# Kernel tuning notes

Hardware: AMD Instinct MI355X
Metric: run time of the kernel (lower is better)

Reference implementation:

```python
import jax, jax.numpy as jnp
import numpy as np

T, N, D, H = 12, 50000, 32, 128  # timesteps, nodes, input_dim, hidden_dim
DEC_STEPS = 7


def setup_inputs() -> dict:
    key = jax.random.key(0)
    ks = jax.random.split(key, 10)
    w = lambda k, shape, s=0.1: jax.random.normal(k, shape, dtype=jnp.float32) * s
    return {
        "x": jax.random.normal(ks[0], (T, N, D), dtype=jnp.float32),
        # input_encoder: Linear(D, H)
        "enc_W": w(ks[1], (H, D)), "enc_b": jnp.zeros((H,), jnp.float32),
        # encoder LSTM (1 layer), PyTorch gate order i,f,g,o
        "Wih_e": w(ks[2], (4 * H, H)), "Whh_e": w(ks[3], (4 * H, H)),
        "bih_e": jnp.zeros((4 * H,), jnp.float32), "bhh_e": jnp.zeros((4 * H,), jnp.float32),
        # decoder LSTM (1 layer)
        "Wih_d": w(ks[4], (4 * H, H)), "Whh_d": w(ks[5], (4 * H, H)),
        "bih_d": jnp.zeros((4 * H,), jnp.float32), "bhh_d": jnp.zeros((4 * H,), jnp.float32),
        # head: fc1(H -> H//2), fc2(H//2 -> 1)
        "fc1_W": w(ks[6], (H // 2, H)), "fc1_b": jnp.zeros((H // 2,), jnp.float32),
        "fc2_W": w(ks[7], (1, H // 2)), "fc2_b": jnp.zeros((1,), jnp.float32),
    }


def _lstm_cell(x, h, c, Wih, Whh, b):
    # PyTorch LSTM gate layout: [i, f, g, o] along the 4H axis.
    z = x @ Wih.T + h @ Whh.T + b
    i, f, g, o = jnp.split(z, 4, axis=-1)
    c = jax.nn.sigmoid(f) * c + jax.nn.sigmoid(i) * jnp.tanh(g)
    h = jax.nn.sigmoid(o) * jnp.tanh(c)
    return h, c


def reference(x, enc_W, enc_b, Wih_e, Whh_e, bih_e, bhh_e,
              Wih_d, Whh_d, bih_d, bhh_d, fc1_W, fc1_b, fc2_W, fc2_b):
    t, n, d = x.shape
    h_dim = enc_W.shape[0]
    # input_encoder applied to all nodes/timesteps at once: [T,N,H]
    enc_seq = jax.nn.relu(jnp.einsum('tnd,hd->tnh', x, enc_W) + enc_b)

    h0 = jnp.zeros((n, h_dim), x.dtype)
    c0 = jnp.zeros((n, h_dim), x.dtype)
    b_e = bih_e + bhh_e

    def enc_step(carry, xt):
        h, c = carry
        h, c = _lstm_cell(xt, h, c, Wih_e, Whh_e, b_e)
        return (h, c), None

    (h, c), _ = jax.lax.scan(enc_step, (h0, c0), enc_seq)

    # decoder input = last encoder output (fixed across all 7 steps, as in source)
    d_in = h
    b_d = bih_d + bhh_d

    def dec_step(carry, _):
        hd, cd = carry
        hd, cd = _lstm_cell(d_in, hd, cd, Wih_d, Whh_d, b_d)
        out = jax.nn.relu(hd @ fc1_W.T + fc1_b)  # dropout is identity at inference
        pred = out @ fc2_W.T + fc2_b             # [N, 1]
        return (hd, cd), pred[:, 0]

    _, preds = jax.lax.scan(dec_step, (h, c), None, length=DEC_STEPS)  # [7, N]
    return preds.T  # [N, 7]
```

## Files before the change

kernel.cpp:

```cpp
#include <hip/hip_runtime.h>

#define TSTEPS 12
#define NNODES 50000
#define DIN 32
#define HDIM 128
#define DECS 7

#define N80 53
#define NB 768
#define RTMAX 5
#define ROWSMAX 80

#define HS 136
#define XS 36
#define ESZ (ROWSMAX * HS)

typedef _Float16 half_t;
typedef _Float16 half8 __attribute__((ext_vector_type(8)));
typedef float float4_ __attribute__((ext_vector_type(4)));

#define WS_FLOAT_OFF 548864

#define SM_BYTES 157440
#define E_OFF 69120
#define H_OFF 112640
#define PRED_OFF 156160
#define ZX_PLANE_H 20480

#if __has_builtin(__builtin_amdgcn_exp2f)
#define EXP2F __builtin_amdgcn_exp2f
#else
#define EXP2F exp2f
#endif
#if __has_builtin(__builtin_amdgcn_rcpf)
#define RCPF __builtin_amdgcn_rcpf
#else
#define RCPF(x) (1.0f / (x))
#endif

__device__ __forceinline__ float lstm_one(float i, float f, float g, float o, float& c) {
    float ai = EXP2F(-1.44269504f * i);
    float af = EXP2F(-1.44269504f * f);
    float ag = EXP2F(-2.88539008f * g);
    float ao = EXP2F(-1.44269504f * o);
    float sf = RCPF(1.0f + af);
    float ig = (1.0f - ag) * RCPF((1.0f + ai) * (1.0f + ag));
    c = fmaf(sf, c, ig);
    float ac = EXP2F(-2.88539008f * c);
    return (1.0f - ac) * RCPF((1.0f + ao) * (1.0f + ac));
}

__global__ void prep_all_k(const float* __restrict__ Wih_e, const float* __restrict__ Whh_e,
                           const float* __restrict__ Wih_d, const float* __restrict__ Whh_d,
                           const float* __restrict__ enc_W, const float* __restrict__ fc1_W,
                           const float* __restrict__ bih_e, const float* __restrict__ bhh_e,
                           const float* __restrict__ bih_d, const float* __restrict__ bhh_d,
                           half_t* __restrict__ wsh, float* __restrict__ be, float* __restrict__ bd) {
    int tid = blockIdx.x * blockDim.x + threadIdx.x;
    if (tid < 262144) {
        int r = tid >> 16;
        int t = tid & 65535;
        const float* src = (r == 0) ? Wih_e : (r == 1) ? Whh_e : (r == 2) ? Wih_d : Whh_d;
        int j    = t & 7;
        int lane = (t >> 3) & 63;
        int rest = t >> 9;
        int kb   = rest & 3;
        int ct   = rest >> 2;
        int row  = ct * 16 + (lane & 15);
        int col  = kb * 32 + ((lane >> 4) << 3) + j;
        wsh[tid] = (half_t)src[row * 128 + col];
    } else if (tid < 266240) {
        int t    = tid - 262144;
        int j    = t & 7;
        int lane = (t >> 3) & 63;
        int ct   = t >> 9;
        int row  = ct * 16 + (lane & 15);
        int col  = ((lane >> 4) << 3) + j;
        wsh[tid] = (half_t)enc_W[row * 32 + col];
    } else if (tid < 274432) {
        int t    = tid - 266240;
        int j    = t & 7;
        int lane = (t >> 3) & 63;
        int rest = t >> 9;
        int kb   = rest & 3;
        int ct   = rest >> 2;
        int row  = ct * 16 + (lane & 15);
        int col  = kb * 32 + ((lane >> 4) << 3) + j;
        wsh[tid] = (half_t)fc1_W[row * 128 + col];
    } else if (tid < 274944) {
        int t = tid - 274432;
        be[t] = bih_e[t] + bhh_e[t];
        bd[t] = bih_d[t] + bhh_d[t];
    }
}

__device__ __forceinline__ void lstm_step(
    const half_t* __restrict__ eA, const half_t* __restrict__ hA, half_t* __restrict__ hOut,
    const half8 (&wfi)[4][4], const half8 (&wfh)[4][4],
    const float bR[4], float (&cS)[RTMAX][4],
    int w, int q, int l15, int RT) {
#pragma unroll
    for (int rt = 0; rt < RTMAX; ++rt) {
        if (rt < RT) {
            float4_ acc[4];
#pragma unroll
            for (int g = 0; g < 4; ++g) {
                float b = bR[g];
                acc[g][0] = b; acc[g][1] = b; acc[g][2] = b; acc[g][3] = b;
            }
#pragma unroll
            for (int kb = 0; kb < 4; ++kb) {
                half8 ae = *(const half8*)(eA + (rt * 16 + l15) * HS + kb * 32 + q * 8);
                half8 ah = *(const half8*)(hA + (rt * 16 + l15) * HS + kb * 32 + q * 8);
#pragma unroll
                for (int g = 0; g < 4; ++g) {
                    acc[g] = __builtin_amdgcn_mfma_f32_16x16x32_f16(ae, wfi[g][kb], acc[g], 0, 0, 0);
                    acc[g] = __builtin_amdgcn_mfma_f32_16x16x32_f16(ah, wfh[g][kb], acc[g], 0, 0, 0);
                }
            }
#pragma unroll
            for (int r = 0; r < 4; ++r) {
                float h = lstm_one(acc[0][r], acc[1][r], acc[2][r], acc[3][r], cS[rt][r]);
                hOut[(rt * 16 + q * 4 + r) * HS + w * 16 + l15] = (half_t)h;
            }
        }
    }
}

__device__ __forceinline__ void lstm_step_dec(
    const half_t* __restrict__ zx, const half_t* __restrict__ hA, half_t* __restrict__ hOut,
    const half8 (&wfh)[4][4], float (&cS)[RTMAX][4],
    int w, int q, int l15, int lane, int RT) {
#pragma unroll
    for (int rt = 0; rt < RTMAX; ++rt) {
        if (rt < RT) {
            const half_t* p0 = zx + ((w * RTMAX + rt) * 64 + lane) * 8;
            half8 z0 = *(const half8*)p0;
            half8 z1 = *(const half8*)(p0 + ZX_PLANE_H);
            float4_ acc[4];
#pragma unroll
            for (int r = 0; r < 4; ++r) {
                acc[0][r] = (float)z0[r];
                acc[1][r] = (float)z0[4 + r];
                acc[2][r] = (float)z1[r];
                acc[3][r] = (float)z1[4 + r];
            }
#pragma unroll
            for (int kb = 0; kb < 4; ++kb) {
                half8 ah = *(const half8*)(hA + (rt * 16 + l15) * HS + kb * 32 + q * 8);
#pragma unroll
                for (int g = 0; g < 4; ++g)
                    acc[g] = __builtin_amdgcn_mfma_f32_16x16x32_f16(ah, wfh[g][kb], acc[g], 0, 0, 0);
            }
#pragma unroll
            for (int r = 0; r < 4; ++r) {
                float h = lstm_one(acc[0][r], acc[1][r], acc[2][r], acc[3][r], cS[rt][r]);
                hOut[(rt * 16 + q * 4 + r) * HS + w * 16 + l15] = (half_t)h;
            }
        }
    }
}

__device__ __forceinline__ void enc_proj(
    const half_t* __restrict__ xa, half_t* __restrict__ eOut,
    half8 encWf, float benc, int t, int w, int q, int l15, int RT) {
#pragma unroll
    for (int rt = 0; rt < RTMAX; ++rt) {
        if (rt < RT) {
            half8 af = *(const half8*)(xa + ((t * ROWSMAX) + rt * 16 + l15) * XS + q * 8);
            float4_ a;
            a[0] = benc; a[1] = benc; a[2] = benc; a[3] = benc;
            a = __builtin_amdgcn_mfma_f32_16x16x32_f16(af, encWf, a, 0, 0, 0);
#pragma unroll
            for (int r = 0; r < 4; ++r) {
                float v = a[r];
                v = v > 0.f ? v : 0.f;
                eOut[(rt * 16 + q * 4 + r) * HS + w * 16 + l15] = (half_t)v;
            }
        }
    }
}

__global__ __launch_bounds__(512, 2) void seq2seq_main_k(
    const float* __restrict__ x,
    const float* __restrict__ enc_b,
    const float* __restrict__ fc1_b,
    const float* __restrict__ fc2_W,
    const float* __restrict__ fc2_b,
    const half_t* __restrict__ wsh,
    const float* __restrict__ be,
    const float* __restrict__ bd,
    float* __restrict__ out) {
    __shared__ __align__(16) char smem[SM_BYTES];
    half_t* xa = (half_t*)smem;
    half_t* eB = (half_t*)(smem + E_OFF);
    half_t* hB = (half_t*)(smem + H_OFF);
    float (*pred)[ROWSMAX] = (float(*)[ROWSMAX])(smem + PRED_OFF);
    half_t* zx = (half_t*)smem;

    const int tid  = threadIdx.x;
    const int lane = tid & 63;
    const int w    = tid >> 6;
    const int q    = lane >> 4;
    const int l15  = lane & 15;
    const int bid  = blockIdx.x;
    const int big  = (bid < N80);
    const int RT   = big ? 5 : 4;
    const int rows = RT << 4;
    const int n0   = big ? bid * 80 : (N80 * 80 + (bid - N80) * 64);

    const half_t* WihE  = wsh;
    const half_t* WhhE  = wsh + 65536;
    const half_t* WihD  = wsh + 131072;
    const half_t* WhhD  = wsh + 196608;
    const half_t* encWp = wsh + 262144;
    const half_t* fc1p  = wsh + 266240;

    float beR[4], bdR[4];
#pragma unroll
    for (int g = 0; g < 4; ++g) {
        int col = g * 128 + w * 16 + l15;
        beR[g] = be[col];
        bdR[g] = bd[col];
    }
    float benc = enc_b[w * 16 + l15];

    for (int it = 0; it < 8; ++it) {
        int unit = tid + it * 512;
        if (unit >= TSTEPS * ROWSMAX * 4) break;
        int t    = unit / (ROWSMAX * 4);
        int rest = unit - t * (ROWSMAX * 4);
        int row  = rest >> 2;
        int c0   = (rest & 3) * 8;
        if (row < rows) {
            const float* p = x + ((size_t)t * NNODES + (n0 + row)) * DIN + c0;
            float4_ a0 = *(const float4_*)p;
            float4_ a1 = *(const float4_*)(p + 4);
            half8 hv;
            hv[0] = (half_t)a0[0]; hv[1] = (half_t)a0[1]; hv[2] = (half_t)a0[2]; hv[3] = (half_t)a0[3];
            hv[4] = (half_t)a1[0]; hv[5] = (half_t)a1[1]; hv[6] = (half_t)a1[2]; hv[7] = (half_t)a1[3];
            *(half8*)(xa + (t * ROWSMAX + row) * XS + c0) = hv;
        }
    }

    for (int i = tid; i < rows * HS; i += 512) hB[i] = (half_t)0.0f;

    float c_reg[RTMAX][4];
#pragma unroll
    for (int rt = 0; rt < RTMAX; ++rt)
#pragma unroll
        for (int r = 0; r < 4; ++r) c_reg[rt][r] = 0.0f;

    half8 wfi[4][4], wfh[4][4];
#pragma unroll
    for (int g = 0; g < 4; ++g)
#pragma unroll
        for (int kb = 0; kb < 4; ++kb) {
            int ct = g * 8 + w;
            wfi[g][kb] = *(const half8*)(WihE + ((size_t)(ct * 4 + kb) * 64 + lane) * 8);
            wfh[g][kb] = *(const half8*)(WhhE + ((size_t)(ct * 4 + kb) * 64 + lane) * 8);
        }
    half8 encWf = *(const half8*)(encWp + (size_t)w * 512 + lane * 8);

    __syncthreads();

    enc_proj(xa, eB, encWf, benc, 0, w, q, l15, RT);
    __syncthreads();

    int cur = 0;
    for (int t = 0; t < TSTEPS; ++t) {
        lstm_step(eB + (t & 1) * ESZ, hB + cur * ESZ, hB + (cur ^ 1) * ESZ,
                  wfi, wfh, beR, c_reg, w, q, l15, RT);
        if (t + 1 < TSTEPS)
            enc_proj(xa, eB + ((t & 1) ^ 1) * ESZ, encWf, benc, t + 1, w, q, l15, RT);
        __syncthreads();
        cur ^= 1;
    }

#pragma unroll
    for (int g = 0; g < 4; ++g)
#pragma unroll
        for (int kb = 0; kb < 4; ++kb) {
            int ct = g * 8 + w;
            wfi[g][kb] = *(const half8*)(WihD + ((size_t)(ct * 4 + kb) * 64 + lane) * 8);
            wfh[g][kb] = *(const half8*)(WhhD + ((size_t)(ct * 4 + kb) * 64 + lane) * 8);
        }
    half8 fc1f[4];
#pragma unroll
    for (int kb = 0; kb < 4; ++kb)
        fc1f[kb] = *(const half8*)(fc1p + ((size_t)((w & 3) * 4 + kb) * 64 + lane) * 8);
    float bf1 = fc1_b[(w & 3) * 16 + l15];
    float wf2 = fc2_W[(w & 3) * 16 + l15];
    float bf2 = fc2_b[0];
    const int gg = w >> 2;

    {
        const half_t* hfin = hB + cur * ESZ;
#pragma unroll
        for (int rt = 0; rt < RTMAX; ++rt) {
            if (rt < RT) {
                float4_ acc[4];
#pragma unroll
                for (int g = 0; g < 4; ++g) {
                    float b = bdR[g];
                    acc[g][0] = b; acc[g][1] = b; acc[g][2] = b; acc[g][3] = b;
                }
#pragma unroll
                for (int kb = 0; kb < 4; ++kb) {
                    half8 ah = *(const half8*)(hfin + (rt * 16 + l15) * HS + kb * 32 + q * 8);
#pragma unroll
                    for (int g = 0; g < 4; ++g)
                        acc[g] = __builtin_amdgcn_mfma_f32_16x16x32_f16(ah, wfi[g][kb], acc[g], 0, 0, 0);
                }
                half8 z0, z1;
#pragma unroll
                for (int r = 0; r < 4; ++r) {
                    z0[r]     = (half_t)acc[0][r];
                    z0[4 + r] = (half_t)acc[1][r];
                    z1[r]     = (half_t)acc[2][r];
                    z1[4 + r] = (half_t)acc[3][r];
                }
                half_t* p0 = zx + ((w * RTMAX + rt) * 64 + lane) * 8;
                *(half8*)p0 = z0;
                *(half8*)(p0 + ZX_PLANE_H) = z1;
            }
        }
    }

    for (int s = 0; s < DECS; ++s) {
        lstm_step_dec(zx, hB + cur * ESZ, hB + (cur ^ 1) * ESZ, wfh, c_reg, w, q, l15, lane, RT);
        cur ^= 1;
        __syncthreads();
        const half_t* hc = hB + cur * ESZ;
#pragma unroll
        for (int rp = 0; rp < 3; ++rp) {
            int rt = gg + rp * 2;
            if (rt < RT) {
                float4_ hacc;
                hacc[0] = bf1; hacc[1] = bf1; hacc[2] = bf1; hacc[3] = bf1;
#pragma unroll
                for (int kb = 0; kb < 4; ++kb) {
                    half8 af = *(const half8*)(hc + (rt * 16 + l15) * HS + kb * 32 + q * 8);
                    hacc = __builtin_amdgcn_mfma_f32_16x16x32_f16(af, fc1f[kb], hacc, 0, 0, 0);
                }
#pragma unroll
                for (int r = 0; r < 4; ++r) {
                    float v = hacc[r];
                    v = v > 0.f ? v : 0.f;
                    v *= wf2;
                    v += __shfl_xor(v, 1, 64);
                    v += __shfl_xor(v, 2, 64);
                    v += __shfl_xor(v, 4, 64);
                    v += __shfl_xor(v, 8, 64);
                    if (l15 == 0) pred[w & 3][rt * 16 + q * 4 + r] = v;
                }
            }
        }
        __syncthreads();
        if (tid < rows) {
            float sum = pred[0][tid] + pred[1][tid] + pred[2][tid] + pred[3][tid] + bf2;
            out[(size_t)(n0 + tid) * DECS + s] = sum;
        }
    }
}

extern "C" void kernel_launch(void* const* d_in, const int* in_sizes, int n_in,
                              void* d_out, int out_size, void* d_ws, size_t ws_size,
                              hipStream_t stream) {
    (void)in_sizes; (void)n_in; (void)out_size; (void)ws_size;
    const float* x     = (const float*)d_in[0];
    const float* enc_W = (const float*)d_in[1];
    const float* enc_b = (const float*)d_in[2];
    const float* Wih_e = (const float*)d_in[3];
    const float* Whh_e = (const float*)d_in[4];
    const float* bih_e = (const float*)d_in[5];
    const float* bhh_e = (const float*)d_in[6];
    const float* Wih_d = (const float*)d_in[7];
    const float* Whh_d = (const float*)d_in[8];
    const float* bih_d = (const float*)d_in[9];
    const float* bhh_d = (const float*)d_in[10];
    const float* fc1_W = (const float*)d_in[11];
    const float* fc1_b = (const float*)d_in[12];
    const float* fc2_W = (const float*)d_in[13];
    const float* fc2_b = (const float*)d_in[14];

    half_t* wsh = (half_t*)d_ws;
    float*  be  = (float*)((char*)d_ws + WS_FLOAT_OFF);
    float*  bd  = be + 512;

    prep_all_k<<<1074, 256, 0, stream>>>(Wih_e, Whh_e, Wih_d, Whh_d, enc_W, fc1_W,
                                         bih_e, bhh_e, bih_d, bhh_d, wsh, be, bd);

    seq2seq_main_k<<<NB, 512, 0, stream>>>(x, enc_b, fc1_b, fc2_W, fc2_b,
                                           wsh, be, bd, (float*)d_out);
}
```

Measured before the change: 419.7 us.

## Fold log2e scaling into LSTM weights, stagger wave phases, raise MFMA priority

The sigmoid/tanh exponent scale factors are folded into the fp16 gate weights and biases during prep, which removes per-element multiplies in the gate nonlinearity and turns one product into an fma. Half of the waves now run the input projection before the LSTM step and swap operand order, so MFMA and VALU work from different waves can interleave. MFMA loops also raise wave priority via s_setprio. The scaling slightly changes fp16 rounding of the weights, and the decoder-side zx path must also use the scaled weights to stay consistent.

```diff
diff --git a/kernel.cpp b/kernel.cpp
--- a/kernel.cpp
+++ b/kernel.cpp
@@ -38,16 +38,18 @@
 #define RCPF(x) (1.0f / (x))
 #endif
 
-__device__ __forceinline__ float lstm_one(float i, float f, float g, float o, float& c) {
-    float ai = EXP2F(-1.44269504f * i);
-    float af = EXP2F(-1.44269504f * f);
-    float ag = EXP2F(-2.88539008f * g);
-    float ao = EXP2F(-1.44269504f * o);
+__device__ __forceinline__ float lstm_one(float zi, float zf, float zg, float zo, float& c) {
+    float ai = EXP2F(-zi);
+    float af = EXP2F(-zf);
+    float ag = EXP2F(-zg);
+    float ao = EXP2F(-zo);
     float sf = RCPF(1.0f + af);
-    float ig = (1.0f - ag) * RCPF((1.0f + ai) * (1.0f + ag));
+    float tg = 1.0f + ag;
+    float ig = (1.0f - ag) * RCPF(fmaf(ai, tg, tg));
     c = fmaf(sf, c, ig);
     float ac = EXP2F(-2.88539008f * c);
-    return (1.0f - ac) * RCPF((1.0f + ao) * (1.0f + ac));
+    float tc = 1.0f + ac;
+    return (1.0f - ac) * RCPF(fmaf(ao, tc, tc));
 }
 
 __global__ void prep_all_k(const float* __restrict__ Wih_e, const float* __restrict__ Whh_e,
@@ -68,7 +70,8 @@
         int ct   = rest >> 2;
         int row  = ct * 16 + (lane & 15);
         int col  = kb * 32 + ((lane >> 4) << 3) + j;
-        wsh[tid] = (half_t)src[row * 128 + col];
+        float scl = ((ct >> 3) == 2) ? 2.8853900818f : 1.4426950409f;
+        wsh[tid] = (half_t)(src[row * 128 + col] * scl);
     } else if (tid < 266240) {
         int t    = tid - 262144;
         int j    = t & 7;
@@ -89,14 +92,15 @@
         wsh[tid] = (half_t)fc1_W[row * 128 + col];
     } else if (tid < 274944) {
         int t = tid - 274432;
-        be[t] = bih_e[t] + bhh_e[t];
-        bd[t] = bih_d[t] + bhh_d[t];
+        float scl = ((t >> 7) == 2) ? 2.8853900818f : 1.4426950409f;
+        be[t] = (bih_e[t] + bhh_e[t]) * scl;
+        bd[t] = (bih_d[t] + bhh_d[t]) * scl;
     }
 }
 
 __device__ __forceinline__ void lstm_step(
     const half_t* __restrict__ eA, const half_t* __restrict__ hA, half_t* __restrict__ hOut,
-    const half8 (&wfi)[4][4], const half8 (&wfh)[4][4],
+    const half8 (&wfA)[4][4], const half8 (&wfB)[4][4],
     const float bR[4], float (&cS)[RTMAX][4],
     int w, int q, int l15, int RT) {
 #pragma unroll
@@ -108,16 +112,18 @@
                 float b = bR[g];
                 acc[g][0] = b; acc[g][1] = b; acc[g][2] = b; acc[g][3] = b;
             }
+            __builtin_amdgcn_s_setprio(1);
 #pragma unroll
             for (int kb = 0; kb < 4; ++kb) {
                 half8 ae = *(const half8*)(eA + (rt * 16 + l15) * HS + kb * 32 + q * 8);
                 half8 ah = *(const half8*)(hA + (rt * 16 + l15) * HS + kb * 32 + q * 8);
 #pragma unroll
                 for (int g = 0; g < 4; ++g) {
-                    acc[g] = __builtin_amdgcn_mfma_f32_16x16x32_f16(ae, wfi[g][kb], acc[g], 0, 0, 0);
-                    acc[g] = __builtin_amdgcn_mfma_f32_16x16x32_f16(ah, wfh[g][kb], acc[g], 0, 0, 0);
-                }
-            }
+                    acc[g] = __builtin_amdgcn_mfma_f32_16x16x32_f16(ae, wfA[g][kb], acc[g], 0, 0, 0);
+                    acc[g] = __builtin_amdgcn_mfma_f32_16x16x32_f16(ah, wfB[g][kb], acc[g], 0, 0, 0);
+                }
+            }
+            __builtin_amdgcn_s_setprio(0);
 #pragma unroll
             for (int r = 0; r < 4; ++r) {
                 float h = lstm_one(acc[0][r], acc[1][r], acc[2][r], acc[3][r], cS[rt][r]);
@@ -145,6 +151,7 @@
                 acc[2][r] = (float)z1[r];
                 acc[3][r] = (float)z1[4 + r];
             }
+            __builtin_amdgcn_s_setprio(1);
 #pragma unroll
             for (int kb = 0; kb < 4; ++kb) {
                 half8 ah = *(const half8*)(hA + (rt * 16 + l15) * HS + kb * 32 + q * 8);
@@ -152,6 +159,7 @@
                 for (int g = 0; g < 4; ++g)
                     acc[g] = __builtin_amdgcn_mfma_f32_16x16x32_f16(ah, wfh[g][kb], acc[g], 0, 0, 0);
             }
+            __builtin_amdgcn_s_setprio(0);
 #pragma unroll
             for (int r = 0; r < 4; ++r) {
                 float h = lstm_one(acc[0][r], acc[1][r], acc[2][r], acc[3][r], cS[rt][r]);
@@ -203,6 +211,7 @@
     const int w    = tid >> 6;
     const int q    = lane >> 4;
     const int l15  = lane & 15;
+    const int ph   = (w >> 2) & 1;
     const int bid  = blockIdx.x;
     const int big  = (bid < N80);
     const int RT   = big ? 5 : 4;
@@ -269,10 +278,19 @@
 
     int cur = 0;
     for (int t = 0; t < TSTEPS; ++t) {
-        lstm_step(eB + (t & 1) * ESZ, hB + cur * ESZ, hB + (cur ^ 1) * ESZ,
-                  wfi, wfh, beR, c_reg, w, q, l15, RT);
-        if (t + 1 < TSTEPS)
-            enc_proj(xa, eB + ((t & 1) ^ 1) * ESZ, encWf, benc, t + 1, w, q, l15, RT);
+        const half_t* eCur  = eB + (t & 1) * ESZ;
+        half_t*       eNext = eB + ((t & 1) ^ 1) * ESZ;
+        const half_t* hCur  = hB + cur * ESZ;
+        half_t*       hNext = hB + (cur ^ 1) * ESZ;
+        if (!ph) {
+            lstm_step(eCur, hCur, hNext, wfi, wfh, beR, c_reg, w, q, l15, RT);
+            if (t + 1 < TSTEPS)
+                enc_proj(xa, eNext, encWf, benc, t + 1, w, q, l15, RT);
+        } else {
+            if (t + 1 < TSTEPS)
+                enc_proj(xa, eNext, encWf, benc, t + 1, w, q, l15, RT);
+            lstm_step(hCur, eCur, hNext, wfh, wfi, beR, c_reg, w, q, l15, RT);
+        }
         __syncthreads();
         cur ^= 1;
     }
```

After: 397.6 us. 1.06x faster.
